# Performance work log

Hardware: AMD Instinct MI355X
Metric: run time of the kernel (lower is better)

Reference implementation:

```python
import jax, jax.numpy as jnp
import numpy as np

N_NODES = 50000
N_EDGES = 400000
HID = 128
EPS_GEN = 1e-7  # GENConv message eps


def layernorm(x, w, b, eps=1e-5):
    mu = x.mean(-1, keepdims=True)
    var = x.var(-1, keepdims=True)
    return (x - mu) / jnp.sqrt(var + eps) * w + b


def segment_softmax(v, seg, n):
    # per-channel softmax over edges sharing the same destination node
    m = jax.ops.segment_max(v, seg, num_segments=n)
    e = jnp.exp(v - m[seg])
    s = jax.ops.segment_sum(e, seg, num_segments=n)
    return e / (s[seg] + 1e-16)


def genconv(x, src, dst, w1, b1, lnw, lnb, w2, b2, t):
    # GENConv(aggr='softmax', t learnable, mlp num_layers=2, norm='layer'), no edge_attr
    n = x.shape[0]
    msg = jax.nn.relu(x[src]) + EPS_GEN            # [E, H]
    alpha = segment_softmax(msg * t, dst, n)       # [E, H]
    aggr = jax.ops.segment_sum(msg * alpha, dst, num_segments=n)  # [N, H]
    h = x + aggr                                   # residual self term
    h = layernorm(h @ w1 + b1, lnw, lnb)           # Linear(H, 2H) + LayerNorm + ReLU
    return jax.nn.relu(h) @ w2 + b2                # Linear(2H, H)


def setup_inputs() -> dict:
    key = jax.random.key(0)
    ks = jax.random.split(key, 30)
    rn = lambda k, shape, s=0.02: jax.random.normal(k, shape, jnp.float32) * s
    inp = {}
    inp['x'] = jax.random.normal(ks[0], (N_NODES, 1024), jnp.float32)
    inp['edge_index'] = jax.random.randint(ks[1], (2, N_EDGES), 0, N_NODES, jnp.int64 if jax.config.jax_enable_x64 else jnp.int32)
    inp['fc_w'] = rn(ks[2], (1024, HID)); inp['fc_b'] = jnp.zeros((HID,), jnp.float32)
    inp['conv_w1'] = rn(ks[3], (3, HID, 2 * HID)); inp['conv_b1'] = jnp.zeros((3, 2 * HID), jnp.float32)
    inp['conv_lnw'] = jnp.ones((3, 2 * HID), jnp.float32); inp['conv_lnb'] = jnp.zeros((3, 2 * HID), jnp.float32)
    inp['conv_w2'] = rn(ks[4], (3, 2 * HID, HID)); inp['conv_b2'] = jnp.zeros((3, HID), jnp.float32)
    inp['conv_t'] = jnp.ones((3,), jnp.float32)
    inp['norm_w'] = jnp.ones((3, HID), jnp.float32); inp['norm_b'] = jnp.zeros((3, HID), jnp.float32)
    D = 4 * HID  # 512
    inp['phi_w'] = rn(ks[5], (D, D)); inp['phi_b'] = jnp.zeros((D,), jnp.float32)
    inp['attn_a_w'] = rn(ks[6], (D, D)); inp['attn_a_b'] = jnp.zeros((D,), jnp.float32)
    inp['attn_b_w'] = rn(ks[7], (D, D)); inp['attn_b_b'] = jnp.zeros((D,), jnp.float32)
    inp['attn_c_w'] = rn(ks[8], (D, 1)); inp['attn_c_b'] = jnp.zeros((1,), jnp.float32)
    inp['rho_w'] = rn(ks[9], (D, D)); inp['rho_b'] = jnp.zeros((D,), jnp.float32)
    inp['cls_w'] = rn(ks[10], (D, 4)); inp['cls_b'] = jnp.zeros((4,), jnp.float32)
    return inp


def reference(x, edge_index, fc_w, fc_b, conv_w1, conv_b1, conv_lnw, conv_lnb,
              conv_w2, conv_b2, conv_t, norm_w, norm_b, phi_w, phi_b,
              attn_a_w, attn_a_b, attn_b_w, attn_b_b, attn_c_w, attn_c_b,
              rho_w, rho_b, cls_w, cls_b):
    src, dst = edge_index[0], edge_index[1]
    # fc (dropout = identity in eval)
    x = jax.nn.relu(x @ fc_w + fc_b)               # [N, 128]
    x_ = x
    # layers[0].conv only (no norm/act/residual)
    x = genconv(x, src, dst, conv_w1[0], conv_b1[0], conv_lnw[0], conv_lnb[0],
                conv_w2[0], conv_b2[0], conv_t[0])
    x_ = jnp.concatenate([x_, x], axis=1)
    # DeepGCNLayer block='res': h = act(norm(conv(x))); x = x + h
    for i in (1, 2):
        h = genconv(x, src, dst, conv_w1[i], conv_b1[i], conv_lnw[i], conv_lnb[i],
                    conv_w2[i], conv_b2[i], conv_t[i])
        h = jax.nn.relu(layernorm(h, norm_w[i], norm_b[i]))
        x = x + h
        x_ = jnp.concatenate([x_, x], axis=1)
    h = jax.nn.relu(x_ @ phi_w + phi_b)            # path_phi, [N, 512]
    a = jnp.tanh(h @ attn_a_w + attn_a_b)
    b = jax.nn.sigmoid(h @ attn_b_w + attn_b_b)
    A = (a * b) @ attn_c_w + attn_c_b              # [N, 1]
    A = jax.nn.softmax(A.T, axis=1)                # [1, N]
    hp = A @ h                                     # [1, 512] attention pooling
    hp = jax.nn.relu(hp @ rho_w + rho_b)[0]        # squeeze -> [512]
    logits = (hp @ cls_w + cls_b)[None, :]         # [1, 4]
    return logits
```

## Files before the change

### kernel.cpp

```cpp
#include <hip/hip_runtime.h>
#include <hip/hip_bf16.h>
#include <math.h>

typedef __bf16 bf16_t;
typedef __attribute__((ext_vector_type(8))) __bf16 bf16x8;
typedef __attribute__((ext_vector_type(2))) __bf16 bf16x2;
typedef __attribute__((ext_vector_type(4))) float f32x4;

__device__ __forceinline__ void gld_lds16(const void* g, void* s) {
    __builtin_amdgcn_global_load_lds(
        (__attribute__((address_space(1))) unsigned int*)g,
        (__attribute__((address_space(3))) unsigned int*)s,
        16, 0, 0);
}

__device__ __forceinline__ int2 sw_decode(int orig, int nwg, int NT) {
    int q = nwg >> 3, r = nwg & 7, xcd = orig & 7, idx = orig >> 3;
    int wg = (xcd < r ? xcd * (q + 1) : r * (q + 1) + (xcd - r) * q) + idx;
    int bx = wg / NT, by = wg - bx * NT;
    return make_int2(bx, by);
}

__device__ __forceinline__ void tconv_tile(const float* __restrict__ in, bf16_t* __restrict__ out,
                                           int R, int C, int rs, int ro, int bx, int by)
{
    __shared__ float tile[32][33];
    int bc = bx * 32, br = by * 32;
    int tx = threadIdx.x & 31, ty = threadIdx.x >> 5;
    #pragma unroll
    for (int i = 0; i < 32; i += 8) {
        int r = br + ty + i, c = bc + tx;
        tile[ty + i][tx] = (r < R && c < C) ? in[(long)r * C + c] : 0.f;
    }
    __syncthreads();
    #pragma unroll
    for (int i = 0; i < 32; i += 8) {
        int c = bc + ty + i, r = br + tx;
        if (c < C && r < R) out[((long)c * rs + ro) * R + r] = (bf16_t)tile[tx][ty + i];
    }
}

__global__ __launch_bounds__(256) void k_prep(const float* __restrict__ fc_w, bf16_t* __restrict__ fcT,
                                              const float* __restrict__ conv_w1, bf16_t* __restrict__ w1T,
                                              const float* __restrict__ conv_w2, bf16_t* __restrict__ w2T,
                                              const float* __restrict__ phi_w, bf16_t* __restrict__ phiT,
                                              const float* __restrict__ aw, const float* __restrict__ bw,
                                              bf16_t* __restrict__ Bcat,
                                              const float* __restrict__ abias, const float* __restrict__ bbias,
                                              float* __restrict__ bias_cat,
                                              int* __restrict__ deg, float* __restrict__ sN,
                                              float* __restrict__ hp, int Nn)
{
    int b = blockIdx.x;
    if (b < 128) {
        tconv_tile(fc_w, fcT, 1024, 128, 1, 0, b & 3, b >> 2);
    } else if (b < 224) {
        int i = (b - 128) >> 5, bb = (b - 128) & 31;
        tconv_tile(conv_w1 + (size_t)i * 128 * 256, w1T + (size_t)i * 256 * 128, 128, 256, 1, 0, bb & 7, bb >> 3);
    } else if (b < 320) {
        int i = (b - 224) >> 5, bb = (b - 224) & 31;
        tconv_tile(conv_w2 + (size_t)i * 256 * 128, w2T + (size_t)i * 128 * 256, 256, 128, 1, 0, bb & 3, bb >> 2);
    } else if (b < 576) {
        int bb = b - 320;
        tconv_tile(phi_w, phiT, 512, 512, 1, 0, bb & 15, bb >> 4);
    } else if (b < 832) {
        int bb = b - 576;
        tconv_tile(aw, Bcat, 512, 512, 2, 0, bb & 15, bb >> 4);
    } else if (b < 1088) {
        int bb = b - 832;
        tconv_tile(bw, Bcat, 512, 512, 2, 1, bb & 15, bb >> 4);
    } else if (b < 1090) {
        int i = (b - 1088) * 256 + threadIdx.x;
        if (i < 512) { bias_cat[2 * i] = abias[i]; bias_cat[2 * i + 1] = bbias[i]; }
    } else if (b < 1286) {
        int i = (b - 1090) * 256 + threadIdx.x;
        if (i < Nn) deg[i] = 0;
    } else if (b < 1482) {
        int i = (b - 1286) * 256 + threadIdx.x;
        if (i < Nn) sN[i] = 0.f;
    } else {
        hp[threadIdx.x] = 0.f;
        hp[threadIdx.x + 256] = 0.f;
    }
}

__global__ __launch_bounds__(256) void k_deg(const int* __restrict__ dst, int* __restrict__ deg, int E)
{
    int e = blockIdx.x * 256 + threadIdx.x;
    if (e < E) atomicAdd(&deg[dst[e]], 1);
}

__global__ __launch_bounds__(1024) void k_scan_a(const int* __restrict__ deg, int* __restrict__ loc,
                                                 int* __restrict__ bsum, int n)
{
    __shared__ int wsum[16];
    int t = threadIdx.x, lane = t & 63, wid = t >> 6;
    int idx = blockIdx.x * 1024 + t;
    int v = (idx < n) ? deg[idx] : 0;
    int x = v;
    #pragma unroll
    for (int d = 1; d < 64; d <<= 1) { int o = __shfl_up(x, d); if (lane >= d) x += o; }
    if (lane == 63) wsum[wid] = x;
    __syncthreads();
    if (wid == 0 && lane < 16) {
        int y = wsum[lane];
        #pragma unroll
        for (int d = 1; d < 16; d <<= 1) { int o = __shfl_up(y, d); if (lane >= d) y += o; }
        wsum[lane] = y;
    }
    __syncthreads();
    int wbase = (wid == 0) ? 0 : wsum[wid - 1];
    if (idx < n) loc[idx] = wbase + x - v;
    if (t == 1023) bsum[blockIdx.x] = wsum[15];
}

__global__ __launch_bounds__(64) void k_scan_b(const int* __restrict__ bsum, int nb,
                                               int* __restrict__ boff, int* __restrict__ off_n)
{
    int lane = threadIdx.x;
    int base = 0;
    for (int c = 0; c < nb; c += 64) {
        int i = c + lane;
        int v = (i < nb) ? bsum[i] : 0;
        int x = v;
        #pragma unroll
        for (int d = 1; d < 64; d <<= 1) { int o = __shfl_up(x, d); if (lane >= d) x += o; }
        if (i < nb) boff[i] = base + x - v;
        base += __shfl(x, 63);
    }
    if (lane == 0) *off_n = base;
}

__global__ __launch_bounds__(1024) void k_scan_c(const int* __restrict__ loc, const int* __restrict__ boff,
                                                 int* __restrict__ off, int* __restrict__ cursor, int n)
{
    int idx = blockIdx.x * 1024 + threadIdx.x;
    if (idx < n) { int v = loc[idx] + boff[blockIdx.x]; off[idx] = v; cursor[idx] = v; }
}

__global__ __launch_bounds__(256) void k_fill(const int* __restrict__ src, const int* __restrict__ dst,
                                              int* __restrict__ cursor, int* __restrict__ csr, int E)
{
    int e = blockIdx.x * 256 + threadIdx.x;
    if (e < E) {
        int d = dst[e];
        int pos = atomicAdd(&cursor[d], 1);
        csr[pos] = src[e];
    }
}

__global__ __launch_bounds__(256) void k_agg(const bf16_t* __restrict__ X,
                                             const int* __restrict__ off, const int* __restrict__ csr,
                                             bf16_t* __restrict__ haux,
                                             const float* __restrict__ tptr, int ti, int Nn)
{
    int w = (blockIdx.x * 256 + threadIdx.x) >> 6;
    if (w >= Nn) return;
    int lane = threadIdx.x & 63;
    float t = tptr[ti];
    int e0 = off[w], e1 = off[w + 1];
    float m0 = -__builtin_inff(), m1 = -__builtin_inff();
    float s0 = 0.f, s1 = 0.f, g0 = 0.f, g1 = 0.f;

    auto proc = [&](bf16x2 xv) {
        float msg0 = fmaxf((float)xv[0], 0.f) + 1e-7f;
        float msg1 = fmaxf((float)xv[1], 0.f) + 1e-7f;
        float v0 = msg0 * t, v1 = msg1 * t;
        if (v0 > m0) { float sc = __expf(m0 - v0); s0 *= sc; g0 *= sc; m0 = v0; }
        float p0 = __expf(v0 - m0); s0 += p0; g0 += msg0 * p0;
        if (v1 > m1) { float sc = __expf(m1 - v1); s1 *= sc; g1 *= sc; m1 = v1; }
        float p1 = __expf(v1 - m1); s1 += p1; g1 += msg1 * p1;
    };

    int e = e0;
    for (; e + 8 <= e1; e += 8) {
        int i0 = csr[e],     i1 = csr[e + 1], i2 = csr[e + 2], i3 = csr[e + 3];
        int i4 = csr[e + 4], i5 = csr[e + 5], i6 = csr[e + 6], i7 = csr[e + 7];
        bf16x2 v0 = *(const bf16x2*)(X + (long)i0 * 128 + lane * 2);
        bf16x2 v1 = *(const bf16x2*)(X + (long)i1 * 128 + lane * 2);
        bf16x2 v2 = *(const bf16x2*)(X + (long)i2 * 128 + lane * 2);
        bf16x2 v3 = *(const bf16x2*)(X + (long)i3 * 128 + lane * 2);
        bf16x2 v4 = *(const bf16x2*)(X + (long)i4 * 128 + lane * 2);
        bf16x2 v5 = *(const bf16x2*)(X + (long)i5 * 128 + lane * 2);
        bf16x2 v6 = *(const bf16x2*)(X + (long)i6 * 128 + lane * 2);
        bf16x2 v7 = *(const bf16x2*)(X + (long)i7 * 128 + lane * 2);
        proc(v0); proc(v1); proc(v2); proc(v3); proc(v4); proc(v5); proc(v6); proc(v7);
    }
    for (; e + 4 <= e1; e += 4) {
        int i0 = csr[e], i1 = csr[e + 1], i2 = csr[e + 2], i3 = csr[e + 3];
        bf16x2 v0 = *(const bf16x2*)(X + (long)i0 * 128 + lane * 2);
        bf16x2 v1 = *(const bf16x2*)(X + (long)i1 * 128 + lane * 2);
        bf16x2 v2 = *(const bf16x2*)(X + (long)i2 * 128 + lane * 2);
        bf16x2 v3 = *(const bf16x2*)(X + (long)i3 * 128 + lane * 2);
        proc(v0); proc(v1); proc(v2); proc(v3);
    }
    for (; e < e1; e++) {
        int s = csr[e];
        bf16x2 xv = *(const bf16x2*)(X + (long)s * 128 + lane * 2);
        proc(xv);
    }
    float a0 = g0 / (s0 + 1e-16f);
    float a1 = g1 / (s1 + 1e-16f);
    bf16x2 xr = *(const bf16x2*)(X + (long)w * 128 + lane * 2);
    bf16_t* outp = haux + (long)w * 128 + lane * 2;
    outp[0] = (bf16_t)((float)xr[0] + a0);
    outp[1] = (bf16_t)((float)xr[1] + a1);
}

template<int BM, int EPI>
__global__ __launch_bounds__(512, 4)
void k_gemm1(const bf16_t* __restrict__ A, int lda,
             const bf16_t* __restrict__ BT,
             const float* __restrict__ bias,
             bf16_t* __restrict__ Cout, int ldc,
             int M, int K, int NT,
             const float* __restrict__ cw,
             float* __restrict__ sout)
{
    constexpr int THREADS = 512;
    constexpr int ACH = BM * 8 / THREADS;
    constexpr int BCH = 128 * 8 / THREADS;
    __shared__ __align__(16) bf16_t lA[BM * 64];
    __shared__ __align__(16) bf16_t lB[128 * 64];
    int2 bxy = sw_decode(blockIdx.x, gridDim.x, NT);
    const int m0 = bxy.x * BM, n0 = bxy.y * 128;
    const int tid = threadIdx.x, lane = tid & 63, wid = tid >> 6;
    const int rbase = (wid >> 1) * 64, cbase = (wid & 1) * 64;
    const int lrow = lane & 15, kg = lane >> 4;
    const int uw = tid & ~63;

    f32x4 acc[4][4];
    #pragma unroll
    for (int m = 0; m < 4; m++)
        #pragma unroll
        for (int n = 0; n < 4; n++)
            #pragma unroll
            for (int r = 0; r < 4; r++) acc[m][n][r] = 0.f;

    auto stage = [&](int k0) {
        #pragma unroll
        for (int c = 0; c < ACH; c++) {
            int s = c * THREADS + tid, row = s >> 3, k8s = (s & 7) ^ (row & 7);
            int gr = m0 + row; gr = gr < M ? gr : M - 1;
            gld_lds16(A + (long)gr * lda + k0 + k8s * 8, lA + (c * THREADS + uw) * 8);
        }
        #pragma unroll
        for (int c = 0; c < BCH; c++) {
            int s = c * THREADS + tid, row = s >> 3, k8s = (s & 7) ^ (row & 7);
            gld_lds16(BT + (long)(n0 + row) * K + k0 + k8s * 8, lB + (c * THREADS + uw) * 8);
        }
    };
    auto compute = [&]() {
        #pragma unroll
        for (int ks = 0; ks < 2; ks++) {
            int k8 = ks * 4 + kg;
            bf16x8 af[4], bfr[4];
            #pragma unroll
            for (int m = 0; m < 4; m++) {
                int r = rbase + m * 16 + lrow;
                af[m] = *(const bf16x8*)&lA[(r * 8 + (k8 ^ (r & 7))) * 8];
            }
            #pragma unroll
            for (int n = 0; n < 4; n++) {
                int r = cbase + n * 16 + lrow;
                bfr[n] = *(const bf16x8*)&lB[(r * 8 + (k8 ^ (r & 7))) * 8];
            }
            #pragma unroll
            for (int m = 0; m < 4; m++)
                #pragma unroll
                for (int n = 0; n < 4; n++)
                    acc[m][n] = __builtin_amdgcn_mfma_f32_16x16x32_bf16(af[m], bfr[n], acc[m][n], 0, 0, 0);
        }
    };

    for (int k0 = 0; k0 < K; k0 += 64) {
        stage(k0);
        __syncthreads();
        compute();
        __syncthreads();
    }

    if constexpr (EPI == 5) {
        #pragma unroll
        for (int m = 0; m < 4; m++) {
            #pragma unroll
            for (int r = 0; r < 4; r++) {
                int row = m0 + rbase + m * 16 + kg * 4 + r;
                float val = 0.f;
                #pragma unroll
                for (int n = 0; n < 4; n++) {
                    int col = n0 + cbase + n * 16 + lrow;
                    float xv = acc[m][n][r] + bias[col];
                    int odd = col & 1;
                    float z = odd ? xv : 2.f * xv;
                    float sg = 1.f / (1.f + __expf(-z));
                    float f = odd ? sg : (2.f * sg - 1.f);
                    float partner = __shfl_xor(f, 1);
                    float prod = f * partner;
                    val += odd ? 0.f : prod * cw[col >> 1];
                }
                #pragma unroll
                for (int o = 1; o < 16; o <<= 1) val += __shfl_xor(val, o);
                if (lrow == 0 && row < M) atomicAdd(&sout[row], val);
            }
        }
    } else {
        #pragma unroll
        for (int m = 0; m < 4; m++) {
            #pragma unroll
            for (int r = 0; r < 4; r++) {
                int row = m0 + rbase + m * 16 + kg * 4 + r;
                if (row >= M) continue;
                #pragma unroll
                for (int n = 0; n < 4; n++) {
                    int col = n0 + cbase + n * 16 + lrow;
                    float xv = fmaxf(acc[m][n][r] + bias[col], 0.f);
                    Cout[(long)row * ldc + col] = (bf16_t)xv;
                }
            }
        }
    }
}

__global__ __launch_bounds__(256) void k_gemm_fcP(const float* __restrict__ Aptr, int lda,
                                                  const bf16_t* __restrict__ BT,
                                                  const float* __restrict__ bias,
                                                  bf16_t* __restrict__ Cout, int ldc,
                                                  bf16_t* __restrict__ Cout2,
                                                  int M, int K)
{
    __shared__ __align__(16) bf16_t lA[128 * 64];
    __shared__ __align__(16) bf16_t lB[128 * 64];
    const int m0 = blockIdx.x * 128;
    const int tid = threadIdx.x, lane = tid & 63, wid = tid >> 6;
    const int rbase = (wid >> 1) * 64, cbase = (wid & 1) * 64;
    const int lrow = lane & 15, kg = lane >> 4;
    const int uw = tid & ~63;

    f32x4 acc[4][4];
    #pragma unroll
    for (int m = 0; m < 4; m++)
        #pragma unroll
        for (int n = 0; n < 4; n++)
            #pragma unroll
            for (int r = 0; r < 4; r++) acc[m][n][r] = 0.f;

    f32x4 fa[8];

    for (int k0 = 0; k0 < K; k0 += 64) {
        #pragma unroll
        for (int c = 0; c < 4; c++) {
            int s = c * 256 + tid, row = s >> 3, k8 = s & 7;
            int gr = m0 + row; gr = gr < M ? gr : M - 1;
            const float* sp = Aptr + (long)gr * lda + k0 + k8 * 8;
            fa[2 * c] = *(const f32x4*)sp;
            fa[2 * c + 1] = *(const f32x4*)(sp + 4);
        }
        #pragma unroll
        for (int c = 0; c < 4; c++) {
            int s = c * 256 + tid, row = s >> 3, k8s = (s & 7) ^ (row & 7);
            gld_lds16(BT + (long)row * K + k0 + k8s * 8, lB + (c * 256 + uw) * 8);
        }
        #pragma unroll
        for (int c = 0; c < 4; c++) {
            int s = c * 256 + tid, row = s >> 3, k8 = s & 7;
            bf16x8 v;
            #pragma unroll
            for (int j = 0; j < 4; j++) { v[j] = (bf16_t)fa[2 * c][j]; v[4 + j] = (bf16_t)fa[2 * c + 1][j]; }
            *(bf16x8*)&lA[(row * 8 + (k8 ^ (row & 7))) * 8] = v;
        }
        __syncthreads();
        #pragma unroll
        for (int ks = 0; ks < 2; ks++) {
            int k8 = ks * 4 + kg;
            bf16x8 af[4], bfr[4];
            #pragma unroll
            for (int m = 0; m < 4; m++) {
                int r = rbase + m * 16 + lrow;
                af[m] = *(const bf16x8*)&lA[(r * 8 + (k8 ^ (r & 7))) * 8];
            }
            #pragma unroll
            for (int n = 0; n < 4; n++) {
                int r = cbase + n * 16 + lrow;
                bfr[n] = *(const bf16x8*)&lB[(r * 8 + (k8 ^ (r & 7))) * 8];
            }
            #pragma unroll
            for (int m = 0; m < 4; m++)
                #pragma unroll
                for (int n = 0; n < 4; n++)
                    acc[m][n] = __builtin_amdgcn_mfma_f32_16x16x32_bf16(af[m], bfr[n], acc[m][n], 0, 0, 0);
        }
        __syncthreads();
    }

    #pragma unroll
    for (int m = 0; m < 4; m++) {
        #pragma unroll
        for (int r = 0; r < 4; r++) {
            int row = m0 + rbase + m * 16 + kg * 4 + r;
            if (row >= M) continue;
            #pragma unroll
            for (int n = 0; n < 4; n++) {
                int col = cbase + n * 16 + lrow;
                float xv = fmaxf(acc[m][n][r] + bias[col], 0.f);
                Cout[(long)row * ldc + col] = (bf16_t)xv;
                Cout2[(long)row * 128 + col] = (bf16_t)xv;
            }
        }
    }
}

template<int MODE>
__global__ __launch_bounds__(512) void k_convf(const bf16_t* __restrict__ A,
                                               const bf16_t* __restrict__ B1T,
                                               const float* __restrict__ b1,
                                               const float* __restrict__ lnw, const float* __restrict__ lnb,
                                               const bf16_t* __restrict__ B2T,
                                               const float* __restrict__ b2,
                                               const float* __restrict__ nw, const float* __restrict__ nb,
                                               const float* __restrict__ xs_in,
                                               bf16_t* __restrict__ xcat_out,
                                               float* __restrict__ xs_out, bf16_t* __restrict__ xl_out,
                                               int M)
{
    __shared__ __align__(16) bf16_t lA[128 * 128];
    __shared__ __align__(16) bf16_t lB1[256 * 128];
    __shared__ __align__(16) bf16_t lB2a[128 * 128];
    bf16_t* h1 = lB1;
    bf16_t* lB2b = lA;

    const int m0 = blockIdx.x * 128;
    const int tid = threadIdx.x, lane = tid & 63, w = tid >> 6;
    const int lrow = lane & 15, kg = lane >> 4;
    const int uw = tid & ~63;

    #pragma unroll
    for (int c = 0; c < 4; c++) {
        int s = c * 512 + tid, row = s >> 4, sl = s & 15;
        int k8 = (sl & 8) | ((sl & 7) ^ (row & 7));
        int gr = m0 + row; gr = gr < M ? gr : M - 1;
        gld_lds16(A + (long)gr * 128 + k8 * 8, lA + (c * 512 + uw) * 8);
    }
    #pragma unroll
    for (int c = 0; c < 8; c++) {
        int s = c * 512 + tid, row = s >> 4, sl = s & 15;
        int k8 = (sl & 8) | ((sl & 7) ^ (row & 7));
        gld_lds16(B1T + (long)row * 128 + k8 * 8, lB1 + (c * 512 + uw) * 8);
    }
    #pragma unroll
    for (int c = 0; c < 4; c++) {
        int s = c * 512 + tid, row = s >> 4, sl = s & 15;
        int k8 = (sl & 8) | ((sl & 7) ^ (row & 7));
        gld_lds16(B2T + (long)row * 256 + k8 * 8, lB2a + (c * 512 + uw) * 8);
    }
    asm volatile("s_waitcnt vmcnt(4)" ::: "memory");
    __builtin_amdgcn_s_barrier();

    f32x4 acc1[16];
    #pragma unroll
    for (int n = 0; n < 16; n++)
        #pragma unroll
        for (int r = 0; r < 4; r++) acc1[n][r] = 0.f;
    #pragma unroll
    for (int ks = 0; ks < 4; ks++) {
        int k8 = ks * 4 + kg;
        int ra = w * 16 + lrow;
        bf16x8 af = *(const bf16x8*)&lA[(ra * 16 + ((k8 & 8) | ((k8 & 7) ^ (ra & 7)))) * 8];
        #pragma unroll
        for (int n = 0; n < 16; n++) {
            int rb = n * 16 + lrow;
            bf16x8 bf = *(const bf16x8*)&lB1[(rb * 16 + ((k8 & 8) | ((k8 & 7) ^ (rb & 7)))) * 8];
            acc1[n] = __builtin_amdgcn_mfma_f32_16x16x32_bf16(af, bf, acc1[n], 0, 0, 0);
        }
    }

    float hv[4][16];
    #pragma unroll
    for (int r = 0; r < 4; r++) {
        float s1 = 0.f, s2 = 0.f;
        #pragma unroll
        for (int n = 0; n < 16; n++) {
            int col = n * 16 + lrow;
            float xv = acc1[n][r] + b1[col];
            hv[r][n] = xv;
            s1 += xv; s2 += xv * xv;
        }
        #pragma unroll
        for (int o = 1; o < 16; o <<= 1) { s1 += __shfl_xor(s1, o); s2 += __shfl_xor(s2, o); }
        float mu = s1 * (1.f / 256.f);
        float var = s2 * (1.f / 256.f) - mu * mu;
        float rstd = rsqrtf(var + 1e-5f);
        #pragma unroll
        for (int n = 0; n < 16; n++) {
            int col = n * 16 + lrow;
            hv[r][n] = fmaxf((hv[r][n] - mu) * rstd * lnw[col] + lnb[col], 0.f);
        }
    }

    __builtin_amdgcn_s_barrier();

    #pragma unroll
    for (int r = 0; r < 4; r++) {
        int row = w * 16 + kg * 4 + r;
        #pragma unroll
        for (int n = 0; n < 16; n++) {
            int col = n * 16 + lrow;
            int chunk = col >> 3;
            int cs = (chunk & 24) | ((chunk & 7) ^ (row & 7));
            h1[row * 256 + cs * 8 + (col & 7)] = (bf16_t)hv[r][n];
        }
    }
    #pragma unroll
    for (int c = 0; c < 4; c++) {
        int s = c * 512 + tid, row = s >> 4, sl = s & 15;
        int k8l = (sl & 8) | ((sl & 7) ^ (row & 7));
        gld_lds16(B2T + (long)row * 256 + (16 + k8l) * 8, lB2b + (c * 512 + uw) * 8);
    }

    f32x4 acc2[8];
    #pragma unroll
    for (int n = 0; n < 8; n++)
        #pragma unroll
        for (int r = 0; r < 4; r++) acc2[n][r] = 0.f;
    #pragma unroll
    for (int ks = 0; ks < 4; ks++) {
        int k8 = ks * 4 + kg;
        int ra = w * 16 + lrow;
        bf16x8 af = *(const bf16x8*)&h1[(ra * 32 + ((k8 & 24) | ((k8 & 7) ^ (ra & 7)))) * 8];
        #pragma unroll
        for (int n = 0; n < 8; n++) {
            int rb = n * 16 + lrow;
            bf16x8 bf = *(const bf16x8*)&lB2a[(rb * 16 + ((k8 & 8) | ((k8 & 7) ^ (rb & 7)))) * 8];
            acc2[n] = __builtin_amdgcn_mfma_f32_16x16x32_bf16(af, bf, acc2[n], 0, 0, 0);
        }
    }
    asm volatile("s_waitcnt vmcnt(0)" ::: "memory");
    __builtin_amdgcn_s_barrier();

    #pragma unroll
    for (int ks = 0; ks < 4; ks++) {
        int k8 = 16 + ks * 4 + kg;
        int k8l = k8 - 16;
        int ra = w * 16 + lrow;
        bf16x8 af = *(const bf16x8*)&h1[(ra * 32 + ((k8 & 24) | ((k8 & 7) ^ (ra & 7)))) * 8];
        #pragma unroll
        for (int n = 0; n < 8; n++) {
            int rb = n * 16 + lrow;
            bf16x8 bf = *(const bf16x8*)&lB2b[(rb * 16 + ((k8l & 8) | ((k8l & 7) ^ (rb & 7)))) * 8];
            acc2[n] = __builtin_amdgcn_mfma_f32_16x16x32_bf16(af, bf, acc2[n], 0, 0, 0);
        }
    }

    #pragma unroll
    for (int r = 0; r < 4; r++) {
        int row = m0 + w * 16 + kg * 4 + r;
        float xv[8];
        #pragma unroll
        for (int n = 0; n < 8; n++) xv[n] = acc2[n][r] + b2[n * 16 + lrow];
        if constexpr (MODE == 1) {
            float s1 = 0.f, s2 = 0.f;
            #pragma unroll
            for (int n = 0; n < 8; n++) { s1 += xv[n]; s2 += xv[n] * xv[n]; }
            #pragma unroll
            for (int o = 1; o < 16; o <<= 1) { s1 += __shfl_xor(s1, o); s2 += __shfl_xor(s2, o); }
            float mu = s1 * (1.f / 128.f);
            float var = s2 * (1.f / 128.f) - mu * mu;
            float rstd = rsqrtf(var + 1e-5f);
            if (row < M) {
                #pragma unroll
                for (int n = 0; n < 8; n++) {
                    int col = n * 16 + lrow;
                    xv[n] = xs_in[(long)row * 128 + col] + fmaxf((xv[n] - mu) * rstd * nw[col] + nb[col], 0.f);
                }
            }
        }
        if (row < M) {
            #pragma unroll
            for (int n = 0; n < 8; n++) {
                int col = n * 16 + lrow;
                xcat_out[(long)row * 512 + col] = (bf16_t)xv[n];
                if (xs_out) xs_out[(long)row * 128 + col] = xv[n];
                if (xl_out) xl_out[(long)row * 128 + col] = (bf16_t)xv[n];
            }
        }
    }
}

__global__ __launch_bounds__(256) void k_sred_a(const float* __restrict__ sN, int Nn,
                                                float* __restrict__ pmax, float* __restrict__ psum)
{
    __shared__ float red[4];
    int t = threadIdx.x, lane = t & 63, wid = t >> 6;
    int stride = gridDim.x * 256;
    float m = -__builtin_inff();
    for (int i = blockIdx.x * 256 + t; i < Nn; i += stride) m = fmaxf(m, sN[i]);
    #pragma unroll
    for (int o = 32; o >= 1; o >>= 1) m = fmaxf(m, __shfl_xor(m, o));
    if (lane == 0) red[wid] = m;
    __syncthreads();
    float bm = fmaxf(fmaxf(red[0], red[1]), fmaxf(red[2], red[3]));
    float s = 0.f;
    for (int i = blockIdx.x * 256 + t; i < Nn; i += stride) s += __expf(sN[i] - bm);
    #pragma unroll
    for (int o = 32; o >= 1; o >>= 1) s += __shfl_xor(s, o);
    __syncthreads();
    if (lane == 0) red[wid] = s;
    __syncthreads();
    if (t == 0) {
        pmax[blockIdx.x] = bm;
        psum[blockIdx.x] = red[0] + red[1] + red[2] + red[3];
    }
}

__global__ __launch_bounds__(64) void k_sred_b(const float* __restrict__ pmax, const float* __restrict__ psum,
                                               int nb, float* __restrict__ red)
{
    int lane = threadIdx.x;
    float m = (lane < nb) ? pmax[lane] : -__builtin_inff();
    #pragma unroll
    for (int o = 32; o >= 1; o >>= 1) m = fmaxf(m, __shfl_xor(m, o));
    float s = (lane < nb) ? psum[lane] * __expf(pmax[lane] - m) : 0.f;
    #pragma unroll
    for (int o = 32; o >= 1; o >>= 1) s += __shfl_xor(s, o);
    if (lane == 0) { red[0] = m; red[1] = s; }
}

__global__ __launch_bounds__(256) void k_pool(const bf16_t* __restrict__ h, const float* __restrict__ sN,
                                              const float* __restrict__ red, float* __restrict__ hp, int Nn)
{
    __shared__ float part[4][512];
    int t = threadIdx.x, lane = t & 63, w = t >> 6;
    float m = red[0], inv = 1.f / red[1];
    float acc[8];
    #pragma unroll
    for (int j = 0; j < 8; j++) acc[j] = 0.f;
    for (int n = blockIdx.x * 4 + w; n < Nn; n += gridDim.x * 4) {
        float wgt = __expf(sN[n] - m) * inv;
        bf16x8 v = *(const bf16x8*)(h + (long)n * 512 + lane * 8);
        #pragma unroll
        for (int j = 0; j < 8; j++) acc[j] += wgt * (float)v[j];
    }
    #pragma unroll
    for (int j = 0; j < 8; j++) part[w][lane * 8 + j] = acc[j];
    __syncthreads();
    #pragma unroll
    for (int c = 0; c < 2; c++) {
        int col = c * 256 + t;
        float s = part[0][col] + part[1][col] + part[2][col] + part[3][col];
        atomicAdd(&hp[col], s);
    }
}

__global__ __launch_bounds__(256) void k_tail_a(const float* __restrict__ hp,
                                                const float* __restrict__ rho_w, const float* __restrict__ rho_b,
                                                float* __restrict__ h2g)
{
    __shared__ float hs[512];
    __shared__ float part[256];
    int t = threadIdx.x;
    hs[t] = hp[t]; hs[t + 256] = hp[t + 256];
    __syncthreads();
    int col = blockIdx.x * 64 + (t & 63);
    int ks = t >> 6;
    float acc = 0.f;
    for (int k = ks * 128; k < ks * 128 + 128; k++) acc += hs[k] * rho_w[(long)k * 512 + col];
    part[t] = acc;
    __syncthreads();
    if (ks == 0) {
        float v = part[t] + part[t + 64] + part[t + 128] + part[t + 192] + rho_b[col];
        h2g[col] = fmaxf(v, 0.f);
    }
}

__global__ __launch_bounds__(256) void k_tail_b(const float* __restrict__ h2g,
                                                const float* __restrict__ cls_w, const float* __restrict__ cls_b,
                                                float* __restrict__ out)
{
    __shared__ float wred[4][4];
    int t = threadIdx.x, lane = t & 63, wid = t >> 6;
    float a0 = 0.f, a1 = 0.f, a2 = 0.f, a3 = 0.f;
    for (int d = t; d < 512; d += 256) {
        float h = h2g[d];
        a0 += h * cls_w[d * 4 + 0];
        a1 += h * cls_w[d * 4 + 1];
        a2 += h * cls_w[d * 4 + 2];
        a3 += h * cls_w[d * 4 + 3];
    }
    #pragma unroll
    for (int o = 32; o >= 1; o >>= 1) {
        a0 += __shfl_xor(a0, o); a1 += __shfl_xor(a1, o);
        a2 += __shfl_xor(a2, o); a3 += __shfl_xor(a3, o);
    }
    if (lane == 0) { wred[wid][0] = a0; wred[wid][1] = a1; wred[wid][2] = a2; wred[wid][3] = a3; }
    __syncthreads();
    if (t < 4)
        out[t] = cls_b[t] + wred[0][t] + wred[1][t] + wred[2][t] + wred[3][t];
}

extern "C" void kernel_launch(void* const* d_in, const int* in_sizes, int n_in,
                              void* d_out, int out_size, void* d_ws, size_t ws_size,
                              hipStream_t stream)
{
    const float* x       = (const float*)d_in[0];
    const int*   eidx    = (const int*)  d_in[1];
    const float* fc_w    = (const float*)d_in[2];
    const float* fc_b    = (const float*)d_in[3];
    const float* conv_w1 = (const float*)d_in[4];
    const float* conv_b1 = (const float*)d_in[5];
    const float* conv_lnw= (const float*)d_in[6];
    const float* conv_lnb= (const float*)d_in[7];
    const float* conv_w2 = (const float*)d_in[8];
    const float* conv_b2 = (const float*)d_in[9];
    const float* conv_t  = (const float*)d_in[10];
    const float* norm_w  = (const float*)d_in[11];
    const float* norm_b  = (const float*)d_in[12];
    const float* phi_w   = (const float*)d_in[13];
    const float* phi_b   = (const float*)d_in[14];
    const float* aw      = (const float*)d_in[15];
    const float* ab      = (const float*)d_in[16];
    const float* bw      = (const float*)d_in[17];
    const float* bb      = (const float*)d_in[18];
    const float* cwp     = (const float*)d_in[19];
    const float* rho_w   = (const float*)d_in[21];
    const float* rho_b   = (const float*)d_in[22];
    const float* cls_w   = (const float*)d_in[23];
    const float* cls_b   = (const float*)d_in[24];

    const int Nn = in_sizes[0] / 1024;
    const int E  = in_sizes[1] / 2;

    char* p = (char*)d_ws;
    auto carve = [&](size_t bytes) { char* r = p; p += (bytes + 255) & ~(size_t)255; return r; };

    bf16_t* x_cat_b = (bf16_t*)carve((size_t)Nn * 512 * 2);
    bf16_t* haux    = (bf16_t*)carve((size_t)Nn * 128 * 2);
    float*  xs1     = (float*)carve((size_t)Nn * 128 * 4);
    float*  xs2     = (float*)carve((size_t)Nn * 128 * 4);
    bf16_t* xl0     = (bf16_t*)carve((size_t)Nn * 128 * 2);
    bf16_t* xl1     = (bf16_t*)carve((size_t)Nn * 128 * 2);
    bf16_t* xl2     = (bf16_t*)carve((size_t)Nn * 128 * 2);
    bf16_t* h_phi   = (bf16_t*)carve((size_t)Nn * 512 * 2);
    bf16_t* fcT  = (bf16_t*)carve((size_t)128 * 1024 * 2);
    bf16_t* w1T  = (bf16_t*)carve((size_t)3 * 256 * 128 * 2);
    bf16_t* w2T  = (bf16_t*)carve((size_t)3 * 128 * 256 * 2);
    bf16_t* phiT = (bf16_t*)carve((size_t)512 * 512 * 2);
    bf16_t* Bcat = (bf16_t*)carve((size_t)1024 * 512 * 2);
    float* bias_cat = (float*)carve(1024 * 4);
    int*   deg    = (int*)carve((size_t)Nn * 4);
    int*   loc    = (int*)carve((size_t)Nn * 4);
    int*   bsum   = (int*)carve(256 * 4);
    int*   boff   = (int*)carve(256 * 4);
    int*   offArr = (int*)carve((size_t)(Nn + 1) * 4);
    int*   cursor = (int*)carve((size_t)Nn * 4);
    int*   csr    = (int*)carve((size_t)E * 4);
    float* sN     = (float*)carve((size_t)Nn * 4);
    float* pmax   = (float*)carve(64 * 4);
    float* psum   = (float*)carve(64 * 4);
    float* red    = (float*)carve(64);
    float* hp     = (float*)carve(512 * 4);
    float* h2g    = (float*)carve(512 * 4);

    const int ZB = (Nn + 255) / 256;
    k_prep<<<1090 + 2 * ZB + 1, 256, 0, stream>>>(fc_w, fcT, conv_w1, w1T, conv_w2, w2T, phi_w, phiT,
                                                  aw, bw, Bcat, ab, bb, bias_cat, deg, sN, hp, Nn);

    const int SB = (Nn + 1023) / 1024;
    k_deg<<<(E + 255) / 256, 256, 0, stream>>>(eidx + E, deg, E);
    k_scan_a<<<SB, 1024, 0, stream>>>(deg, loc, bsum, Nn);
    k_scan_b<<<1, 64, 0, stream>>>(bsum, SB, boff, offArr + Nn);
    k_scan_c<<<SB, 1024, 0, stream>>>(loc, boff, offArr, cursor, Nn);
    k_fill<<<(E + 255) / 256, 256, 0, stream>>>(eidx, eidx + E, cursor, csr, E);

    const int MT128 = (Nn + 127) / 128;
    const int MT256 = (Nn + 255) / 256;
    const int agB = (Nn + 3) / 4;

    k_gemm_fcP<<<MT128, 256, 0, stream>>>(x, 1024, fcT, fc_b, x_cat_b, 512, xl0, Nn, 1024);

    const bf16_t* xls[3] = {xl0, xl1, xl2};
    for (int i = 0; i < 3; i++) {
        k_agg<<<agB, 256, 0, stream>>>(xls[i], offArr, csr, haux, conv_t, i, Nn);
        if (i == 0)
            k_convf<0><<<MT128, 512, 0, stream>>>(haux, w1T, conv_b1, conv_lnw, conv_lnb,
                                                  w2T, conv_b2, nullptr, nullptr, nullptr,
                                                  x_cat_b + 128, xs1, xl1, Nn);
        else if (i == 1)
            k_convf<1><<<MT128, 512, 0, stream>>>(haux, w1T + (size_t)256 * 128, conv_b1 + 256,
                                                  conv_lnw + 256, conv_lnb + 256,
                                                  w2T + (size_t)128 * 256, conv_b2 + 128,
                                                  norm_w + 128, norm_b + 128, xs1,
                                                  x_cat_b + 256, xs2, xl2, Nn);
        else
            k_convf<1><<<MT128, 512, 0, stream>>>(haux, w1T + (size_t)2 * 256 * 128, conv_b1 + 512,
                                                  conv_lnw + 512, conv_lnb + 512,
                                                  w2T + (size_t)2 * 128 * 256, conv_b2 + 256,
                                                  norm_w + 256, norm_b + 256, xs2,
                                                  x_cat_b + 384, nullptr, nullptr, Nn);
    }

    k_gemm1<256, 3><<<MT256 * 4, 512, 0, stream>>>(x_cat_b, 512, phiT, phi_b, h_phi, 512,
                                                   Nn, 512, 4, nullptr, nullptr);
    k_gemm1<256, 5><<<MT256 * 8, 512, 0, stream>>>(h_phi, 512, Bcat, bias_cat, nullptr, 0,
                                                   Nn, 512, 8, cwp, sN);
    k_sred_a<<<64, 256, 0, stream>>>(sN, Nn, pmax, psum);
    k_sred_b<<<1, 64, 0, stream>>>(pmax, psum, 64, red);
    k_pool<<<256, 256, 0, stream>>>(h_phi, sN, red, hp, Nn);
    k_tail_a<<<8, 256, 0, stream>>>(hp, rho_w, rho_b, h2g);
    k_tail_b<<<1, 256, 0, stream>>>(h2g, cls_w, cls_b, (float*)d_out);
}
```

Measured before the change: 563.8 us.

## Fuse softmax edge aggregation into the GENConv MLP kernel

Removes the separate k_agg kernel. Each k_convf block now computes the softmax-weighted neighbor aggregation plus residual for its 128 rows, one wave per 16 rows, and writes the result straight into the swizzled LDS A tile. This drops the haux round-trip through global memory and one launch per layer, while the weight loads into LDS overlap the gather. The trade-off is that the gather now runs with the GEMM kernel's occupancy, which is limited by its large LDS footprint. That could expose more gather latency than the standalone kernel did, which had many more waves in flight.

```diff
diff --git a/kernel.cpp b/kernel.cpp
--- a/kernel.cpp
+++ b/kernel.cpp
@@ -149,64 +149,6 @@
     }
 }
 
-__global__ __launch_bounds__(256) void k_agg(const bf16_t* __restrict__ X,
-                                             const int* __restrict__ off, const int* __restrict__ csr,
-                                             bf16_t* __restrict__ haux,
-                                             const float* __restrict__ tptr, int ti, int Nn)
-{
-    int w = (blockIdx.x * 256 + threadIdx.x) >> 6;
-    if (w >= Nn) return;
-    int lane = threadIdx.x & 63;
-    float t = tptr[ti];
-    int e0 = off[w], e1 = off[w + 1];
-    float m0 = -__builtin_inff(), m1 = -__builtin_inff();
-    float s0 = 0.f, s1 = 0.f, g0 = 0.f, g1 = 0.f;
-
-    auto proc = [&](bf16x2 xv) {
-        float msg0 = fmaxf((float)xv[0], 0.f) + 1e-7f;
-        float msg1 = fmaxf((float)xv[1], 0.f) + 1e-7f;
-        float v0 = msg0 * t, v1 = msg1 * t;
-        if (v0 > m0) { float sc = __expf(m0 - v0); s0 *= sc; g0 *= sc; m0 = v0; }
-        float p0 = __expf(v0 - m0); s0 += p0; g0 += msg0 * p0;
-        if (v1 > m1) { float sc = __expf(m1 - v1); s1 *= sc; g1 *= sc; m1 = v1; }
-        float p1 = __expf(v1 - m1); s1 += p1; g1 += msg1 * p1;
-    };
-
-    int e = e0;
-    for (; e + 8 <= e1; e += 8) {
-        int i0 = csr[e],     i1 = csr[e + 1], i2 = csr[e + 2], i3 = csr[e + 3];
-        int i4 = csr[e + 4], i5 = csr[e + 5], i6 = csr[e + 6], i7 = csr[e + 7];
-        bf16x2 v0 = *(const bf16x2*)(X + (long)i0 * 128 + lane * 2);
-        bf16x2 v1 = *(const bf16x2*)(X + (long)i1 * 128 + lane * 2);
-        bf16x2 v2 = *(const bf16x2*)(X + (long)i2 * 128 + lane * 2);
-        bf16x2 v3 = *(const bf16x2*)(X + (long)i3 * 128 + lane * 2);
-        bf16x2 v4 = *(const bf16x2*)(X + (long)i4 * 128 + lane * 2);
-        bf16x2 v5 = *(const bf16x2*)(X + (long)i5 * 128 + lane * 2);
-        bf16x2 v6 = *(const bf16x2*)(X + (long)i6 * 128 + lane * 2);
-        bf16x2 v7 = *(const bf16x2*)(X + (long)i7 * 128 + lane * 2);
-        proc(v0); proc(v1); proc(v2); proc(v3); proc(v4); proc(v5); proc(v6); proc(v7);
-    }
-    for (; e + 4 <= e1; e += 4) {
-        int i0 = csr[e], i1 = csr[e + 1], i2 = csr[e + 2], i3 = csr[e + 3];
-        bf16x2 v0 = *(const bf16x2*)(X + (long)i0 * 128 + lane * 2);
-        bf16x2 v1 = *(const bf16x2*)(X + (long)i1 * 128 + lane * 2);
-        bf16x2 v2 = *(const bf16x2*)(X + (long)i2 * 128 + lane * 2);
-        bf16x2 v3 = *(const bf16x2*)(X + (long)i3 * 128 + lane * 2);
-        proc(v0); proc(v1); proc(v2); proc(v3);
-    }
-    for (; e < e1; e++) {
-        int s = csr[e];
-        bf16x2 xv = *(const bf16x2*)(X + (long)s * 128 + lane * 2);
-        proc(xv);
-    }
-    float a0 = g0 / (s0 + 1e-16f);
-    float a1 = g1 / (s1 + 1e-16f);
-    bf16x2 xr = *(const bf16x2*)(X + (long)w * 128 + lane * 2);
-    bf16_t* outp = haux + (long)w * 128 + lane * 2;
-    outp[0] = (bf16_t)((float)xr[0] + a0);
-    outp[1] = (bf16_t)((float)xr[1] + a1);
-}
-
 template<int BM, int EPI>
 __global__ __launch_bounds__(512, 4)
 void k_gemm1(const bf16_t* __restrict__ A, int lda,
@@ -411,7 +353,9 @@
 }
 
 template<int MODE>
-__global__ __launch_bounds__(512) void k_convf(const bf16_t* __restrict__ A,
+__global__ __launch_bounds__(512) void k_convf(const bf16_t* __restrict__ X,
+                                               const int* __restrict__ off, const int* __restrict__ csr,
+                                               const float* __restrict__ tptr, int ti,
                                                const bf16_t* __restrict__ B1T,
                                                const float* __restrict__ b1,
                                                const float* __restrict__ lnw, const float* __restrict__ lnb,
@@ -435,13 +379,6 @@
     const int uw = tid & ~63;
 
     #pragma unroll
-    for (int c = 0; c < 4; c++) {
-        int s = c * 512 + tid, row = s >> 4, sl = s & 15;
-        int k8 = (sl & 8) | ((sl & 7) ^ (row & 7));
-        int gr = m0 + row; gr = gr < M ? gr : M - 1;
-        gld_lds16(A + (long)gr * 128 + k8 * 8, lA + (c * 512 + uw) * 8);
-    }
-    #pragma unroll
     for (int c = 0; c < 8; c++) {
         int s = c * 512 + tid, row = s >> 4, sl = s & 15;
         int k8 = (sl & 8) | ((sl & 7) ^ (row & 7));
@@ -453,7 +390,66 @@
         int k8 = (sl & 8) | ((sl & 7) ^ (row & 7));
         gld_lds16(B2T + (long)row * 256 + k8 * 8, lB2a + (c * 512 + uw) * 8);
     }
-    asm volatile("s_waitcnt vmcnt(4)" ::: "memory");
+    asm volatile("" ::: "memory");
+
+    {
+        float t = tptr[ti];
+        for (int rr = 0; rr < 16; rr++) {
+            int lr = w * 16 + rr;
+            int grow = m0 + lr; grow = grow < M ? grow : M - 1;
+            int e0 = off[grow], e1 = off[grow + 1];
+            float mm0 = -__builtin_inff(), mm1 = -__builtin_inff();
+            float s0 = 0.f, s1 = 0.f, g0 = 0.f, g1 = 0.f;
+
+            auto proc = [&](bf16x2 xv) {
+                float msg0 = fmaxf((float)xv[0], 0.f) + 1e-7f;
+                float msg1 = fmaxf((float)xv[1], 0.f) + 1e-7f;
+                float v0 = msg0 * t, v1 = msg1 * t;
+                if (v0 > mm0) { float sc = __expf(mm0 - v0); s0 *= sc; g0 *= sc; mm0 = v0; }
+                float p0 = __expf(v0 - mm0); s0 += p0; g0 += msg0 * p0;
+                if (v1 > mm1) { float sc = __expf(mm1 - v1); s1 *= sc; g1 *= sc; mm1 = v1; }
+                float p1 = __expf(v1 - mm1); s1 += p1; g1 += msg1 * p1;
+            };
+
+            int e = e0;
+            for (; e + 8 <= e1; e += 8) {
+                int i0 = csr[e],     i1 = csr[e + 1], i2 = csr[e + 2], i3 = csr[e + 3];
+                int i4 = csr[e + 4], i5 = csr[e + 5], i6 = csr[e + 6], i7 = csr[e + 7];
+                bf16x2 v0 = *(const bf16x2*)(X + (long)i0 * 128 + lane * 2);
+                bf16x2 v1 = *(const bf16x2*)(X + (long)i1 * 128 + lane * 2);
+                bf16x2 v2 = *(const bf16x2*)(X + (long)i2 * 128 + lane * 2);
+                bf16x2 v3 = *(const bf16x2*)(X + (long)i3 * 128 + lane * 2);
+                bf16x2 v4 = *(const bf16x2*)(X + (long)i4 * 128 + lane * 2);
+                bf16x2 v5 = *(const bf16x2*)(X + (long)i5 * 128 + lane * 2);
+                bf16x2 v6 = *(const bf16x2*)(X + (long)i6 * 128 + lane * 2);
+                bf16x2 v7 = *(const bf16x2*)(X + (long)i7 * 128 + lane * 2);
+                proc(v0); proc(v1); proc(v2); proc(v3); proc(v4); proc(v5); proc(v6); proc(v7);
+            }
+            for (; e + 4 <= e1; e += 4) {
+                int i0 = csr[e], i1 = csr[e + 1], i2 = csr[e + 2], i3 = csr[e + 3];
+                bf16x2 v0 = *(const bf16x2*)(X + (long)i0 * 128 + lane * 2);
+                bf16x2 v1 = *(const bf16x2*)(X + (long)i1 * 128 + lane * 2);
+                bf16x2 v2 = *(const bf16x2*)(X + (long)i2 * 128 + lane * 2);
+                bf16x2 v3 = *(const bf16x2*)(X + (long)i3 * 128 + lane * 2);
+                proc(v0); proc(v1); proc(v2); proc(v3);
+            }
+            for (; e < e1; e++) {
+                int s = csr[e];
+                bf16x2 xv = *(const bf16x2*)(X + (long)s * 128 + lane * 2);
+                proc(xv);
+            }
+            float a0 = g0 / (s0 + 1e-16f);
+            float a1 = g1 / (s1 + 1e-16f);
+            bf16x2 xr = *(const bf16x2*)(X + (long)grow * 128 + lane * 2);
+            int c0 = lane * 2;
+            int chunk = c0 >> 3;
+            int cs = (chunk & 8) | ((chunk & 7) ^ (lr & 7));
+            bf16x2 ob; ob[0] = (bf16_t)((float)xr[0] + a0); ob[1] = (bf16_t)((float)xr[1] + a1);
+            *(bf16x2*)&lA[lr * 128 + cs * 8 + (c0 & 7)] = ob;
+        }
+    }
+
+    asm volatile("s_waitcnt vmcnt(0)" ::: "memory");
     __builtin_amdgcn_s_barrier();
 
     f32x4 acc1[16];
@@ -733,7 +729,6 @@
     auto carve = [&](size_t bytes) { char* r = p; p += (bytes + 255) & ~(size_t)255; return r; };
 
     bf16_t* x_cat_b = (bf16_t*)carve((size_t)Nn * 512 * 2);
-    bf16_t* haux    = (bf16_t*)carve((size_t)Nn * 128 * 2);
     float*  xs1     = (float*)carve((size_t)Nn * 128 * 4);
     float*  xs2     = (float*)carve((size_t)Nn * 128 * 4);
     bf16_t* xl0     = (bf16_t*)carve((size_t)Nn * 128 * 2);
@@ -773,30 +768,25 @@
 
     const int MT128 = (Nn + 127) / 128;
     const int MT256 = (Nn + 255) / 256;
-    const int agB = (Nn + 3) / 4;
 
     k_gemm_fcP<<<MT128, 256, 0, stream>>>(x, 1024, fcT, fc_b, x_cat_b, 512, xl0, Nn, 1024);
 
-    const bf16_t* xls[3] = {xl0, xl1, xl2};
-    for (int i = 0; i < 3; i++) {
-        k_agg<<<agB, 256, 0, stream>>>(xls[i], offArr, csr, haux, conv_t, i, Nn);
-        if (i == 0)
-            k_convf<0><<<MT128, 512, 0, stream>>>(haux, w1T, conv_b1, conv_lnw, conv_lnb,
-                                                  w2T, conv_b2, nullptr, nullptr, nullptr,
-                                                  x_cat_b + 128, xs1, xl1, Nn);
-        else if (i == 1)
-            k_convf<1><<<MT128, 512, 0, stream>>>(haux, w1T + (size_t)256 * 128, conv_b1 + 256,
-                                                  conv_lnw + 256, conv_lnb + 256,
-                                                  w2T + (size_t)128 * 256, conv_b2 + 128,
-                                                  norm_w + 128, norm_b + 128, xs1,
-                                                  x_cat_b + 256, xs2, xl2, Nn);
-        else
-            k_convf<1><<<MT128, 512, 0, stream>>>(haux, w1T + (size_t)2 * 256 * 128, conv_b1 + 512,
-                                                  conv_lnw + 512, conv_lnb + 512,
-                                                  w2T + (size_t)2 * 128 * 256, conv_b2 + 256,
-                                                  norm_w + 256, norm_b + 256, xs2,
-                                                  x_cat_b + 384, nullptr, nullptr, Nn);
-    }
+    k_convf<0><<<MT128, 512, 0, stream>>>(xl0, offArr, csr, conv_t, 0,
+                                          w1T, conv_b1, conv_lnw, conv_lnb,
+                                          w2T, conv_b2, nullptr, nullptr, nullptr,
+                                          x_cat_b + 128, xs1, xl1, Nn);
+    k_convf<1><<<MT128, 512, 0, stream>>>(xl1, offArr, csr, conv_t, 1,
+                                          w1T + (size_t)256 * 128, conv_b1 + 256,
+                                          conv_lnw + 256, conv_lnb + 256,
+                                          w2T + (size_t)128 * 256, conv_b2 + 128,
+                                          norm_w + 128, norm_b + 128, xs1,
+                                          x_cat_b + 256, xs2, xl2, Nn);
+    k_convf<1><<<MT128, 512, 0, stream>>>(xl2, offArr, csr, conv_t, 2,
+                                          w1T + (size_t)2 * 256 * 128, conv_b1 + 512,
+                                          conv_lnw + 512, conv_lnb + 512,
+                                          w2T + (size_t)2 * 128 * 256, conv_b2 + 256,
+                                          norm_w + 256, norm_b + 256, xs2,
+                                          x_cat_b + 384, nullptr, nullptr, Nn);
 
     k_gemm1<256, 3><<<MT256 * 4, 512, 0, stream>>>(x_cat_b, 512, phiT, phi_b, h_phi, 512,
                                                    Nn, 512, 4, nullptr, nullptr);
```

Result: slower. 708.1 us (+25.6%).
